# Performance work log

Hardware: AMD Instinct MI355X
Metric: run time of the kernel (lower is better)

## Reference

```python
import jax, jax.numpy as jnp
import numpy as np

LAMBDA_CHAMFER = 1.0
LAMBDA_EDGE = 0.1


def setup_inputs() -> dict:
    key = jax.random.key(0)
    k1, k2, k3 = jax.random.split(key, 3)
    B, N, M, E = 8, 4096, 4096, 12288
    pred_vertices = jax.random.normal(k1, (B, N, 3), dtype=jnp.float32)
    gt_vertices = jax.random.normal(k2, (B, M, 3), dtype=jnp.float32)
    edges = jax.random.randint(k3, (E, 2), 0, N, dtype=jnp.int64)
    return {"pred_vertices": pred_vertices, "gt_vertices": gt_vertices, "edges": edges}


def _pairwise_dist(p1, p2):
    # ||x - y|| computed via the expanded form to avoid a [B,N,M,3] intermediate.
    # dist2[b,n,m] = |p1[b,n]|^2 + |p2[b,m]|^2 - 2 * p1[b,n] . p2[b,m]
    sq1 = jnp.sum(p1 * p1, axis=-1)  # [B, N]
    sq2 = jnp.sum(p2 * p2, axis=-1)  # [B, M]
    cross = jnp.einsum('bnd,bmd->bnm', p1, p2)  # [B, N, M]
    dist2 = sq1[:, :, None] + sq2[:, None, :] - 2.0 * cross
    return jnp.sqrt(jnp.maximum(dist2, 0.0))


def chamfer_distance(p1, p2):
    dist = _pairwise_dist(p1, p2)  # [B, N, M]
    min_p1 = jnp.min(dist, axis=2)  # [B, N] nearest gt for each pred point
    min_p2 = jnp.min(dist, axis=1)  # [B, M] nearest pred for each gt point
    return jnp.mean(min_p1) + jnp.mean(min_p2)


def edge_length_regularization(vertices, edges):
    v1 = vertices[:, edges[:, 0]]  # [B, E, 3]
    v2 = vertices[:, edges[:, 1]]  # [B, E, 3]
    lengths = jnp.linalg.norm(v1 - v2, axis=2)  # [B, E]
    return jnp.var(lengths, ddof=1)  # torch.var is unbiased by default


def reference(pred_vertices, gt_vertices, edges):
    cd = chamfer_distance(pred_vertices, gt_vertices)
    edge_loss = edge_length_regularization(pred_vertices, edges)
    return LAMBDA_CHAMFER * cd + LAMBDA_EDGE * edge_loss
```

## Files before the change

### kernel.cpp

```cpp
#include <hip/hip_runtime.h>
#include <hip/hip_bf16.h>
#include <float.h>

constexpr int B = 8, N = 4096, M = 4096, E = 12288;
constexpr int TB = 512;
constexpr int EDGE_BLOCKS = (B * E) / TB;
constexpr int SWEEP_BLOCKS = B * 16 * 2;
constexpr size_t BFRAG = 0;
constexpr size_t ROWP  = 262144;
constexpr size_t COLP  = 327680;
constexpr size_t EOFF  = 851968;
constexpr size_t SUMS  = 852352;

typedef short bf16x8  __attribute__((ext_vector_type(8)));
typedef float f32x16  __attribute__((ext_vector_type(16)));

__device__ __forceinline__ unsigned short f2bf(float x) {
    unsigned u = __float_as_uint(x);
    unsigned r = u + 0x7FFFu + ((u >> 16) & 1u);
    return (unsigned short)(r >> 16);
}
__device__ __forceinline__ float bf2f(unsigned short h) {
    return __uint_as_float(((unsigned)h) << 16);
}
constexpr unsigned short BF_ONE = 0x3F80;

__global__ __launch_bounds__(256) void pack_kernel(
    const float* __restrict__ gt, unsigned short* __restrict__ bfrag) {
    const int i = blockIdx.x * 256 + threadIdx.x;
    const float* p = gt + (size_t)i * 3;
    const float x = p[0], y = p[1], z = p[2];
    const unsigned short hx = f2bf(x), hy = f2bf(y), hz = f2bf(z);
    const float fx = bf2f(hx), fy = bf2f(hy), fz = bf2f(hz);
    const unsigned short lx = f2bf(x - fx), ly = f2bf(y - fy), lz = f2bf(z - fz);
    const float c = x * x + y * y + z * z;
    const unsigned short ch = f2bf(c);
    const unsigned short cl = f2bf(c - bf2f(ch));
    const unsigned short ax = f2bf(-2.f * fx), bx = f2bf(-2.f * bf2f(lx));
    const unsigned short ay = f2bf(-2.f * fy), by = f2bf(-2.f * bf2f(ly));
    const unsigned short az = f2bf(-2.f * fz), bz = f2bf(-2.f * bf2f(lz));

    unsigned short* d0 = bfrag + (size_t)(((i >> 5) * 64) + (i & 31)) * 8;
    unsigned short* d1 = d0 + 32 * 8;
    d0[0] = ax; d0[1] = ax; d0[2] = bx; d0[3] = bx;
    d0[4] = ay; d0[5] = ay; d0[6] = by; d0[7] = by;
    d1[0] = az; d1[1] = az; d1[2] = bz; d1[3] = bz;
    d1[4] = ch; d1[5] = cl; d1[6] = BF_ONE; d1[7] = BF_ONE;
}

__global__ __launch_bounds__(TB) void sweep_kernel(
    const float* __restrict__ pred, const unsigned short* __restrict__ bfrag,
    const int* __restrict__ edges, float* __restrict__ wsf) {
    const int bid = blockIdx.x;
    const int t = threadIdx.x;
    __shared__ unsigned colmin[2048];
    __shared__ float wsum[8], wsum2[8];

    if (bid >= EDGE_BLOCKS) {
        const int sb   = bid - EDGE_BLOCKS;
        const int b    = sb >> 5;
        const int nblk = (sb & 31) >> 1;
        const int mh   = sb & 1;
        const int wv = t >> 6, l = t & 63;
        const int nt = nblk * 8 + wv;

        for (int i = t; i < 2048; i += TB) colmin[i] = 0xFFFFFFFFu;

        const float* qp = pred + ((size_t)b * N + nt * 32 + (l & 31)) * 3;
        const float x = qp[0], y = qp[1], z = qp[2];
        const unsigned short hx = f2bf(x), hy = f2bf(y), hz = f2bf(z);
        const unsigned short lx = f2bf(x - bf2f(hx));
        const unsigned short ly = f2bf(y - bf2f(hy));
        const unsigned short lz = f2bf(z - bf2f(hz));
        const float d = x * x + y * y + z * z;
        const unsigned short dh = f2bf(d);
        const unsigned short dl = f2bf(d - bf2f(dh));
        bf16x8 af;
        if (l < 32) {
            af[0] = (short)hx; af[1] = (short)lx; af[2] = (short)hx; af[3] = (short)lx;
            af[4] = (short)hy; af[5] = (short)ly; af[6] = (short)hy; af[7] = (short)ly;
        } else {
            af[0] = (short)hz; af[1] = (short)lz; af[2] = (short)hz; af[3] = (short)lz;
            af[4] = (short)BF_ONE; af[5] = (short)BF_ONE; af[6] = (short)dh; af[7] = (short)dl;
        }
        __syncthreads();

        const unsigned short* bp =
            bfrag + ((size_t)((b * 128 + mh * 64) * 64) + l) * 8;
        float rowacc[16];
#pragma unroll
        for (int r = 0; r < 16; ++r) rowacc[r] = FLT_MAX;
        f32x16 zacc = {};

        bf16x8 bcur = *(const bf16x8*)bp;
        for (int mt = 0; mt < 64; ++mt) {
            const int nx = (mt + 1 < 64) ? mt + 1 : 63;
            bf16x8 bnxt = *(const bf16x8*)(bp + (size_t)nx * 512);
            f32x16 D = __builtin_amdgcn_mfma_f32_32x32x16_bf16(af, bcur, zacc, 0, 0, 0);
#pragma unroll
            for (int r = 0; r < 16; ++r) rowacc[r] = fminf(rowacc[r], D[r]);
            float t1, t2, t3, t4, t5, u1, u2;
            asm("v_min3_f32 %0, %1, %2, %3" : "=v"(t1) : "v"(D[0]),  "v"(D[1]),  "v"(D[2]));
            asm("v_min3_f32 %0, %1, %2, %3" : "=v"(t2) : "v"(D[3]),  "v"(D[4]),  "v"(D[5]));
            asm("v_min3_f32 %0, %1, %2, %3" : "=v"(t3) : "v"(D[6]),  "v"(D[7]),  "v"(D[8]));
            asm("v_min3_f32 %0, %1, %2, %3" : "=v"(t4) : "v"(D[9]),  "v"(D[10]), "v"(D[11]));
            asm("v_min3_f32 %0, %1, %2, %3" : "=v"(t5) : "v"(D[12]), "v"(D[13]), "v"(D[14]));
            asm("v_min3_f32 %0, %1, %2, %3" : "=v"(u1) : "v"(t1), "v"(t2), "v"(t3));
            asm("v_min3_f32 %0, %1, %2, %3" : "=v"(u2) : "v"(t4), "v"(t5), "v"(D[15]));
            float colv = fminf(u1, u2);
            colv = fminf(colv, __shfl_xor(colv, 32, 64));
            atomicMin(&colmin[mt * 32 + (l & 31)], __float_as_uint(fmaxf(colv, 0.f)));
            bcur = bnxt;
        }

#pragma unroll
        for (int r = 0; r < 16; ++r) {
            float v = rowacc[r];
            v = fminf(v, __shfl_xor(v, 1, 64));
            v = fminf(v, __shfl_xor(v, 2, 64));
            v = fminf(v, __shfl_xor(v, 4, 64));
            v = fminf(v, __shfl_xor(v, 8, 64));
            v = fminf(v, __shfl_xor(v, 16, 64));
            rowacc[r] = v;
        }
        if ((l & 31) == 0) {
            float* rp = wsf + ROWP + ((size_t)(b * 2 + mh) * 128 + nt) * 32;
            const int hb = (l >> 5) * 4;
#pragma unroll
            for (int r = 0; r < 16; ++r)
                rp[(r & 3) + 8 * (r >> 2) + hb] = fmaxf(rowacc[r], 0.f);
        }
        __syncthreads();
        float* cp = wsf + COLP + (size_t)((b * 2 + mh) * 16 + nblk) * 2048;
        for (int i = t; i < 2048; i += TB)
            cp[i] = __uint_as_float(colmin[i]);
    } else {
        const int eg = bid * TB + t;
        const int b  = eg / E;
        const int e  = eg - b * E;
        const int i0 = edges[2 * e], i1 = edges[2 * e + 1];
        const float* p0 = pred + ((size_t)b * N + i0) * 3;
        const float* p1 = pred + ((size_t)b * N + i1) * 3;
        const float dx = p0[0] - p1[0];
        const float dy = p0[1] - p1[1];
        const float dz = p0[2] - p1[2];
        float L  = sqrtf(dx * dx + dy * dy + dz * dz);
        float L2 = L * L;
#pragma unroll
        for (int o = 32; o > 0; o >>= 1) {
            L  += __shfl_down(L, o, 64);
            L2 += __shfl_down(L2, o, 64);
        }
        const int wv = t >> 6;
        if ((t & 63) == 0) { wsum[wv] = L; wsum2[wv] = L2; }
        __syncthreads();
        if (t == 0) {
            float a = 0.0f, c = 0.0f;
#pragma unroll
            for (int w = 0; w < 8; w++) { a += wsum[w]; c += wsum2[w]; }
            wsf[EOFF + 2 * bid]     = a;
            wsf[EOFF + 2 * bid + 1] = c;
        }
    }
}

__global__ __launch_bounds__(512) void final1_kernel(
    const float* __restrict__ wsf, float* __restrict__ sums) {
    const int g = blockIdx.x * 512 + threadIdx.x;
    const int b = g >> 12, i = g & 4095;
    const int mh = i >> 11, ci = i & 2047;
    const float* cp = wsf + COLP + (size_t)((b * 2 + mh) * 16) * 2048 + ci;
    float cm = cp[0];
#pragma unroll
    for (int k = 1; k < 16; ++k) cm = fminf(cm, cp[(size_t)k * 2048]);
    const float* rp = wsf + ROWP + (size_t)b * 2 * 4096 + i;
    const float rm = fminf(rp[0], rp[4096]);
    float sv = sqrtf(cm) + sqrtf(rm);
#pragma unroll
    for (int o = 32; o > 0; o >>= 1) sv += __shfl_down(sv, o, 64);
    __shared__ float w[8];
    if ((threadIdx.x & 63) == 0) w[threadIdx.x >> 6] = sv;
    __syncthreads();
    if (threadIdx.x == 0) {
        float s = 0.f;
#pragma unroll
        for (int k = 0; k < 8; ++k) s += w[k];
        sums[blockIdx.x] = s;
    }
}

__global__ __launch_bounds__(256) void final2_kernel(
    const float* __restrict__ wsf, const float* __restrict__ sums,
    float* __restrict__ out) {
    const int t = threadIdx.x;
    float sc = (t < 64) ? sums[t] : 0.f;
    float s1 = 0.f, s2 = 0.f;
    if (t < EDGE_BLOCKS) {
        s1 = wsf[EOFF + 2 * t];
        s2 = wsf[EOFF + 2 * t + 1];
    }
#pragma unroll
    for (int o = 32; o > 0; o >>= 1) {
        sc += __shfl_down(sc, o, 64);
        s1 += __shfl_down(s1, o, 64);
        s2 += __shfl_down(s2, o, 64);
    }
    __shared__ float w[3][4];
    const int wv = t >> 6, ln = t & 63;
    if (ln == 0) { w[0][wv] = sc; w[1][wv] = s1; w[2][wv] = s2; }
    __syncthreads();
    if (t == 0) {
        float S = 0.f, A = 0.f, C = 0.f;
#pragma unroll
        for (int i = 0; i < 4; i++) { S += w[0][i]; A += w[1][i]; C += w[2][i]; }
        const float K = (float)(B * E);
        const float var = (C - A * A / K) / (K - 1.0f);
        out[0] = S / 32768.0f + 0.1f * var;
    }
}

extern "C" void kernel_launch(void* const* d_in, const int* in_sizes, int n_in,
                              void* d_out, int out_size, void* d_ws, size_t ws_size,
                              hipStream_t stream) {
    const float* pred  = (const float*)d_in[0];
    const float* gt    = (const float*)d_in[1];
    const int*   edges = (const int*)d_in[2];
    float* out = (float*)d_out;
    float* wsf = (float*)d_ws;
    unsigned short* bfrag = (unsigned short*)d_ws;
    float* sums = wsf + SUMS;

    pack_kernel<<<(B * M) / 256, 256, 0, stream>>>(gt, bfrag);
    sweep_kernel<<<EDGE_BLOCKS + SWEEP_BLOCKS, TB, 0, stream>>>(pred, bfrag, edges, wsf);
    final1_kernel<<<64, 512, 0, stream>>>(wsf, sums);
    final2_kernel<<<1, 256, 0, stream>>>(wsf, sums, out);
}
```

Baseline: 86.20 us.

## Compute chamfer as two symmetric row-min sweeps instead of row+column atomics

Replaces the single pred×gt sweep, which tracked column minima via LDS atomicMin per tile, with two symmetric sweeps (pred vs gt and gt vs pred). Each takes only row minima over all 128 column tiles. This removes the per-tile min3 tree, the cross-lane shuffle, the LDS atomics and the column partial buffers. The price is doubled MFMA work and a second packed operand set. The two final reduction kernels are also merged into one 1024-thread kernel.

```diff
diff --git a/kernel.cpp b/kernel.cpp
--- a/kernel.cpp
+++ b/kernel.cpp
@@ -5,12 +5,9 @@
 constexpr int B = 8, N = 4096, M = 4096, E = 12288;
 constexpr int TB = 512;
 constexpr int EDGE_BLOCKS = (B * E) / TB;
-constexpr int SWEEP_BLOCKS = B * 16 * 2;
-constexpr size_t BFRAG = 0;
-constexpr size_t ROWP  = 262144;
-constexpr size_t COLP  = 327680;
-constexpr size_t EOFF  = 851968;
-constexpr size_t SUMS  = 852352;
+constexpr int SWEEP_BLOCKS = 2 * B * 16;
+constexpr size_t MINV = 524288;
+constexpr size_t EOFF = 589824;
 
 typedef short bf16x8  __attribute__((ext_vector_type(8)));
 typedef float f32x16  __attribute__((ext_vector_type(16)));
@@ -26,55 +23,62 @@
 constexpr unsigned short BF_ONE = 0x3F80;
 
 __global__ __launch_bounds__(256) void pack_kernel(
-    const float* __restrict__ gt, unsigned short* __restrict__ bfrag) {
-    const int i = blockIdx.x * 256 + threadIdx.x;
-    const float* p = gt + (size_t)i * 3;
+    const float* __restrict__ pred, const float* __restrict__ gt,
+    unsigned short* __restrict__ bfrag) {
+    const int i  = blockIdx.x * 256 + threadIdx.x;
+    const int cc = i >> 15;
+    const int j  = i & 32767;
+    const float* p = (cc ? gt : pred) + (size_t)j * 3;
     const float x = p[0], y = p[1], z = p[2];
     const unsigned short hx = f2bf(x), hy = f2bf(y), hz = f2bf(z);
-    const float fx = bf2f(hx), fy = bf2f(hy), fz = bf2f(hz);
-    const unsigned short lx = f2bf(x - fx), ly = f2bf(y - fy), lz = f2bf(z - fz);
+    const unsigned short lx = f2bf(x - bf2f(hx));
+    const unsigned short ly = f2bf(y - bf2f(hy));
+    const unsigned short lz = f2bf(z - bf2f(hz));
     const float c = x * x + y * y + z * z;
     const unsigned short ch = f2bf(c);
     const unsigned short cl = f2bf(c - bf2f(ch));
-    const unsigned short ax = f2bf(-2.f * fx), bx = f2bf(-2.f * bf2f(lx));
-    const unsigned short ay = f2bf(-2.f * fy), by = f2bf(-2.f * bf2f(ly));
-    const unsigned short az = f2bf(-2.f * fz), bz = f2bf(-2.f * bf2f(lz));
-
-    unsigned short* d0 = bfrag + (size_t)(((i >> 5) * 64) + (i & 31)) * 8;
-    unsigned short* d1 = d0 + 32 * 8;
-    d0[0] = ax; d0[1] = ax; d0[2] = bx; d0[3] = bx;
-    d0[4] = ay; d0[5] = ay; d0[6] = by; d0[7] = by;
-    d1[0] = az; d1[1] = az; d1[2] = bz; d1[3] = bz;
-    d1[4] = ch; d1[5] = cl; d1[6] = BF_ONE; d1[7] = BF_ONE;
+    const unsigned short ax = f2bf(-2.f * bf2f(hx)), bx = f2bf(-2.f * bf2f(lx));
+    const unsigned short ay = f2bf(-2.f * bf2f(hy)), by = f2bf(-2.f * bf2f(ly));
+    const unsigned short az = f2bf(-2.f * bf2f(hz)), bz = f2bf(-2.f * bf2f(lz));
+
+    bf16x8 v0, v1;
+    v0[0] = (short)ax; v0[1] = (short)ax; v0[2] = (short)bx; v0[3] = (short)bx;
+    v0[4] = (short)ay; v0[5] = (short)ay; v0[6] = (short)by; v0[7] = (short)by;
+    v1[0] = (short)az; v1[1] = (short)az; v1[2] = (short)bz; v1[3] = (short)bz;
+    v1[4] = (short)ch; v1[5] = (short)cl; v1[6] = (short)BF_ONE; v1[7] = (short)BF_ONE;
+
+    unsigned short* base =
+        bfrag + (size_t)cc * 524288 + ((size_t)(j >> 5) * 64 + (j & 31)) * 8;
+    *(bf16x8*)base         = v0;
+    *(bf16x8*)(base + 256) = v1;
 }
 
 __global__ __launch_bounds__(TB) void sweep_kernel(
-    const float* __restrict__ pred, const unsigned short* __restrict__ bfrag,
-    const int* __restrict__ edges, float* __restrict__ wsf) {
+    const float* __restrict__ pred, const float* __restrict__ gt,
+    const unsigned short* __restrict__ bfrag, const int* __restrict__ edges,
+    float* __restrict__ wsf) {
     const int bid = blockIdx.x;
     const int t = threadIdx.x;
-    __shared__ unsigned colmin[2048];
     __shared__ float wsum[8], wsum2[8];
 
     if (bid >= EDGE_BLOCKS) {
-        const int sb   = bid - EDGE_BLOCKS;
-        const int b    = sb >> 5;
-        const int nblk = (sb & 31) >> 1;
-        const int mh   = sb & 1;
+        const int sb = bid - EDGE_BLOCKS;
+        const int d  = sb >> 7;
+        const int b  = (sb >> 4) & 7;
+        const int ng = sb & 15;
         const int wv = t >> 6, l = t & 63;
-        const int nt = nblk * 8 + wv;
-
-        for (int i = t; i < 2048; i += TB) colmin[i] = 0xFFFFFFFFu;
-
-        const float* qp = pred + ((size_t)b * N + nt * 32 + (l & 31)) * 3;
+        const int nt = ng * 8 + wv;
+
+        const float* qsrc = d ? gt : pred;
+        const float* qp = qsrc + (size_t)(b * 4096 + nt * 32 + (l & 31)) * 3;
         const float x = qp[0], y = qp[1], z = qp[2];
         const unsigned short hx = f2bf(x), hy = f2bf(y), hz = f2bf(z);
         const unsigned short lx = f2bf(x - bf2f(hx));
         const unsigned short ly = f2bf(y - bf2f(hy));
         const unsigned short lz = f2bf(z - bf2f(hz));
-        const float d = x * x + y * y + z * z;
-        const unsigned short dh = f2bf(d);
-        const unsigned short dl = f2bf(d - bf2f(dh));
+        const float dd = x * x + y * y + z * z;
+        const unsigned short dh = f2bf(dd);
+        const unsigned short dl = f2bf(dd - bf2f(dh));
         bf16x8 af;
         if (l < 32) {
             af[0] = (short)hx; af[1] = (short)lx; af[2] = (short)hx; af[3] = (short)lx;
@@ -83,34 +87,24 @@
             af[0] = (short)hz; af[1] = (short)lz; af[2] = (short)hz; af[3] = (short)lz;
             af[4] = (short)BF_ONE; af[5] = (short)BF_ONE; af[6] = (short)dh; af[7] = (short)dl;
         }
-        __syncthreads();
 
         const unsigned short* bp =
-            bfrag + ((size_t)((b * 128 + mh * 64) * 64) + l) * 8;
+            bfrag + (size_t)(1 - d) * 524288 + ((size_t)(b * 128) * 64 + l) * 8;
         float rowacc[16];
 #pragma unroll
         for (int r = 0; r < 16; ++r) rowacc[r] = FLT_MAX;
         f32x16 zacc = {};
 
-        bf16x8 bcur = *(const bf16x8*)bp;
-        for (int mt = 0; mt < 64; ++mt) {
-            const int nx = (mt + 1 < 64) ? mt + 1 : 63;
-            bf16x8 bnxt = *(const bf16x8*)(bp + (size_t)nx * 512);
-            f32x16 D = __builtin_amdgcn_mfma_f32_32x32x16_bf16(af, bcur, zacc, 0, 0, 0);
+        bf16x8 b0 = *(const bf16x8*)bp;
+        bf16x8 b1 = *(const bf16x8*)(bp + 512);
+#pragma unroll 2
+        for (int mt = 0; mt < 128; ++mt) {
+            bf16x8 bn = b1;
+            if (mt + 2 < 128) bn = *(const bf16x8*)(bp + (size_t)(mt + 2) * 512);
+            const f32x16 D = __builtin_amdgcn_mfma_f32_32x32x16_bf16(af, b0, zacc, 0, 0, 0);
 #pragma unroll
             for (int r = 0; r < 16; ++r) rowacc[r] = fminf(rowacc[r], D[r]);
-            float t1, t2, t3, t4, t5, u1, u2;
-            asm("v_min3_f32 %0, %1, %2, %3" : "=v"(t1) : "v"(D[0]),  "v"(D[1]),  "v"(D[2]));
-            asm("v_min3_f32 %0, %1, %2, %3" : "=v"(t2) : "v"(D[3]),  "v"(D[4]),  "v"(D[5]));
-            asm("v_min3_f32 %0, %1, %2, %3" : "=v"(t3) : "v"(D[6]),  "v"(D[7]),  "v"(D[8]));
-            asm("v_min3_f32 %0, %1, %2, %3" : "=v"(t4) : "v"(D[9]),  "v"(D[10]), "v"(D[11]));
-            asm("v_min3_f32 %0, %1, %2, %3" : "=v"(t5) : "v"(D[12]), "v"(D[13]), "v"(D[14]));
-            asm("v_min3_f32 %0, %1, %2, %3" : "=v"(u1) : "v"(t1), "v"(t2), "v"(t3));
-            asm("v_min3_f32 %0, %1, %2, %3" : "=v"(u2) : "v"(t4), "v"(t5), "v"(D[15]));
-            float colv = fminf(u1, u2);
-            colv = fminf(colv, __shfl_xor(colv, 32, 64));
-            atomicMin(&colmin[mt * 32 + (l & 31)], __float_as_uint(fmaxf(colv, 0.f)));
-            bcur = bnxt;
+            b0 = b1; b1 = bn;
         }
 
 #pragma unroll
@@ -124,16 +118,12 @@
             rowacc[r] = v;
         }
         if ((l & 31) == 0) {
-            float* rp = wsf + ROWP + ((size_t)(b * 2 + mh) * 128 + nt) * 32;
+            float* rp = wsf + MINV + (size_t)(d * 8 + b) * 4096 + (size_t)nt * 32;
             const int hb = (l >> 5) * 4;
 #pragma unroll
             for (int r = 0; r < 16; ++r)
                 rp[(r & 3) + 8 * (r >> 2) + hb] = fmaxf(rowacc[r], 0.f);
         }
-        __syncthreads();
-        float* cp = wsf + COLP + (size_t)((b * 2 + mh) * 16 + nblk) * 2048;
-        for (int i = t; i < 2048; i += TB)
-            cp[i] = __uint_as_float(colmin[i]);
     } else {
         const int eg = bid * TB + t;
         const int b  = eg / E;
@@ -164,37 +154,14 @@
     }
 }
 
-__global__ __launch_bounds__(512) void final1_kernel(
-    const float* __restrict__ wsf, float* __restrict__ sums) {
-    const int g = blockIdx.x * 512 + threadIdx.x;
-    const int b = g >> 12, i = g & 4095;
-    const int mh = i >> 11, ci = i & 2047;
-    const float* cp = wsf + COLP + (size_t)((b * 2 + mh) * 16) * 2048 + ci;
-    float cm = cp[0];
-#pragma unroll
-    for (int k = 1; k < 16; ++k) cm = fminf(cm, cp[(size_t)k * 2048]);
-    const float* rp = wsf + ROWP + (size_t)b * 2 * 4096 + i;
-    const float rm = fminf(rp[0], rp[4096]);
-    float sv = sqrtf(cm) + sqrtf(rm);
-#pragma unroll
-    for (int o = 32; o > 0; o >>= 1) sv += __shfl_down(sv, o, 64);
-    __shared__ float w[8];
-    if ((threadIdx.x & 63) == 0) w[threadIdx.x >> 6] = sv;
-    __syncthreads();
-    if (threadIdx.x == 0) {
-        float s = 0.f;
-#pragma unroll
-        for (int k = 0; k < 8; ++k) s += w[k];
-        sums[blockIdx.x] = s;
-    }
-}
-
-__global__ __launch_bounds__(256) void final2_kernel(
-    const float* __restrict__ wsf, const float* __restrict__ sums,
-    float* __restrict__ out) {
+__global__ __launch_bounds__(1024) void final_kernel(
+    const float* __restrict__ wsf, float* __restrict__ out) {
     const int t = threadIdx.x;
-    float sc = (t < 64) ? sums[t] : 0.f;
-    float s1 = 0.f, s2 = 0.f;
+    float sc = 0.0f;
+#pragma unroll 8
+    for (int k = 0; k < 64; ++k)
+        sc += sqrtf(wsf[MINV + t + (size_t)k * 1024]);
+    float s1 = 0.0f, s2 = 0.0f;
     if (t < EDGE_BLOCKS) {
         s1 = wsf[EOFF + 2 * t];
         s2 = wsf[EOFF + 2 * t + 1];
@@ -205,14 +172,14 @@
         s1 += __shfl_down(s1, o, 64);
         s2 += __shfl_down(s2, o, 64);
     }
-    __shared__ float w[3][4];
+    __shared__ float w[3][16];
     const int wv = t >> 6, ln = t & 63;
     if (ln == 0) { w[0][wv] = sc; w[1][wv] = s1; w[2][wv] = s2; }
     __syncthreads();
     if (t == 0) {
         float S = 0.f, A = 0.f, C = 0.f;
 #pragma unroll
-        for (int i = 0; i < 4; i++) { S += w[0][i]; A += w[1][i]; C += w[2][i]; }
+        for (int i = 0; i < 16; i++) { S += w[0][i]; A += w[1][i]; C += w[2][i]; }
         const float K = (float)(B * E);
         const float var = (C - A * A / K) / (K - 1.0f);
         out[0] = S / 32768.0f + 0.1f * var;
@@ -228,10 +195,8 @@
     float* out = (float*)d_out;
     float* wsf = (float*)d_ws;
     unsigned short* bfrag = (unsigned short*)d_ws;
-    float* sums = wsf + SUMS;
-
-    pack_kernel<<<(B * M) / 256, 256, 0, stream>>>(gt, bfrag);
-    sweep_kernel<<<EDGE_BLOCKS + SWEEP_BLOCKS, TB, 0, stream>>>(pred, bfrag, edges, wsf);
-    final1_kernel<<<64, 512, 0, stream>>>(wsf, sums);
-    final2_kernel<<<1, 256, 0, stream>>>(wsf, sums, out);
-}
+
+    pack_kernel<<<256, 256, 0, stream>>>(pred, gt, bfrag);
+    sweep_kernel<<<EDGE_BLOCKS + SWEEP_BLOCKS, TB, 0, stream>>>(pred, gt, bfrag, edges, wsf);
+    final_kernel<<<1, 1024, 0, stream>>>(wsf, out);
+}
```

New measurement: 106.5 us. 23.5% more time.
